# Kernel optimization log

Hardware: AMD Instinct MI355X
Metric: run time of the kernel (lower is better)

Reference implementation:

```python
import jax, jax.numpy as jnp
import numpy as np

N, EG, T, H, EC, L, NT = 10000, 200000, 300000, 128, 128, 3, 100


def _ssp(x):
    # ShiftedSoftplus: softplus(x) - log(2)
    return jax.nn.softplus(x) - jnp.log(2.0).astype(x.dtype)


def _bn(x, g, b):
    # BatchNorm1d in training mode: biased batch stats, eps=1e-5
    m = jnp.mean(x, axis=0)
    v = jnp.var(x, axis=0)
    return g * (x - m) * jax.lax.rsqrt(v + 1e-5) + b


def _forward(z, i, j, idx_i, idx_j, idx_k, idx_ji, idx_kj, pos,
             We1, be1, We2, be2, We3, be3,
             Wc1, bc1, g_c1, b_c1, g_n, b_n,
             Wc2, bc2, g_c2, b_c2, Wc3, bc3, g_c3, b_c3,
             g_c22, b_c22, g_c32, b_c32,
             Wf1, bf1, Wf2, bf2, Wf3, bf3):
    # AtomType2NodeEmb
    h = jax.nn.one_hot(z, NT, dtype=jnp.float32)
    h = _ssp(h @ We1 + be1)
    h = _ssp(h @ We2 + be2)
    node = h @ We3 + be3                      # [N, H]
    # geometry + GaussianFilter edge embedding
    rel = pos[i] - pos[j]                     # [EG, 3]
    dist = jnp.sqrt(jnp.sum(rel * rel, axis=-1))
    unit = rel / dist[:, None]
    offset = jnp.linspace(0.0, 5.0, EC)
    coeff = -0.5 / (offset[1] - offset[0]) ** 2
    edge = jnp.exp(coeff * (dist[:, None] - offset[None, :]) ** 2)  # [EG, EC]
    for l in range(L):
        # NodeUpdate
        c1 = jnp.concatenate([node[i], edge], axis=1) @ Wc1[l] + bc1[l]
        c1 = _bn(c1, g_c1[l], b_c1[l])
        f1, r1 = jnp.split(c1, 2, axis=1)
        agg = jax.ops.segment_sum(jax.nn.sigmoid(f1) * jnp.tanh(r1), i, num_segments=N)
        node = jnp.tanh(node + _bn(agg, g_n[l], b_n[l]))
        # EdgeUpdate: pair term
        c2 = (node[i] * node[j]) @ Wc2[l] + bc2[l]
        c2 = _bn(c2, g_c2[l], b_c2[l])
        f2, r2 = jnp.split(c2, 2, axis=1)
        c2_emb = _bn(jax.nn.sigmoid(f2) * jnp.tanh(r2), g_c22[l], b_c22[l])
        # EdgeUpdate: triplet term
        c3 = jnp.concatenate([node[idx_i], node[idx_j], node[idx_k],
                              edge[idx_ji], edge[idx_kj]], axis=1) @ Wc3[l] + bc3[l]
        c3 = _bn(c3, g_c3[l], b_c3[l])
        f3, r3 = jnp.split(c3, 2, axis=1)
        agg3 = jax.ops.segment_sum(jax.nn.sigmoid(f3) * jnp.tanh(r3), idx_ji, num_segments=EG)
        c3_emb = _bn(agg3, g_c32[l], b_c32[l])
        edge = jnp.tanh(edge + c2_emb + c3_emb)
    # ForcePredictor
    f = _ssp(edge @ Wf1 + bf1)
    f = _ssp(f @ Wf2 + bf2)
    force = (f @ Wf3 + bf3) * unit            # [EG, 3]
    return jax.ops.segment_sum(force, i, num_segments=N)


def setup_inputs() -> dict:
    ks = iter(jax.random.split(jax.random.key(0), 32))

    def w(shape):
        return jax.random.normal(next(ks), shape, jnp.float32) * (shape[-2] ** -0.5)

    z = jax.random.randint(next(ks), (N,), 0, NT)
    pos = jax.random.uniform(next(ks), (N, 3), jnp.float32) * 5.0
    i = jax.random.randint(next(ks), (EG,), 0, N)
    j = (i + 1 + jax.random.randint(next(ks), (EG,), 0, N - 1)) % N  # no self-loops
    idx_i = jax.random.randint(next(ks), (T,), 0, N)
    idx_j = jax.random.randint(next(ks), (T,), 0, N)
    idx_k = jax.random.randint(next(ks), (T,), 0, N)
    idx_ji = jax.random.randint(next(ks), (T,), 0, EG)
    idx_kj = jax.random.randint(next(ks), (T,), 0, EG)
    return dict(
        z=z, pos=pos, i=i, j=j, idx_i=idx_i, idx_j=idx_j, idx_k=idx_k,
        idx_ji=idx_ji, idx_kj=idx_kj,
        We1=w((NT, H)), be1=jnp.zeros((H,)), We2=w((H, H)), be2=jnp.zeros((H,)),
        We3=w((H, H)), be3=jnp.zeros((H,)),
        Wc1=w((L, H + EC, 2 * H)), bc1=jnp.zeros((L, 2 * H)),
        g_c1=jnp.ones((L, 2 * H)), b_c1=jnp.zeros((L, 2 * H)),
        g_n=jnp.ones((L, H)), b_n=jnp.zeros((L, H)),
        Wc2=w((L, H, 2 * EC)), bc2=jnp.zeros((L, 2 * EC)),
        g_c2=jnp.ones((L, 2 * EC)), b_c2=jnp.zeros((L, 2 * EC)),
        Wc3=w((L, 3 * H + 2 * EC, 2 * EC)), bc3=jnp.zeros((L, 2 * EC)),
        g_c3=jnp.ones((L, 2 * EC)), b_c3=jnp.zeros((L, 2 * EC)),
        g_c22=jnp.ones((L, EC)), b_c22=jnp.zeros((L, EC)),
        g_c32=jnp.ones((L, EC)), b_c32=jnp.zeros((L, EC)),
        Wf1=w((EC, EC)), bf1=jnp.zeros((EC,)), Wf2=w((EC, EC)), bf2=jnp.zeros((EC,)),
        Wf3=w((EC, 1)), bf3=jnp.zeros((1,)),
    )


def reference(z, pos, i, j, idx_i, idx_j, idx_k, idx_ji, idx_kj,
              We1, be1, We2, be2, We3, be3,
              Wc1, bc1, g_c1, b_c1, g_n, b_n,
              Wc2, bc2, g_c2, b_c2, Wc3, bc3, g_c3, b_c3,
              g_c22, b_c22, g_c32, b_c32,
              Wf1, bf1, Wf2, bf2, Wf3, bf3):
    return _forward(z, i, j, idx_i, idx_j, idx_k, idx_ji, idx_kj, pos,
                    We1, be1, We2, be2, We3, be3,
                    Wc1, bc1, g_c1, b_c1, g_n, b_n,
                    Wc2, bc2, g_c2, b_c2, Wc3, bc3, g_c3, b_c3,
                    g_c22, b_c22, g_c32, b_c32,
                    Wf1, bf1, Wf2, bf2, Wf3, bf3)
```

## Files before the change

### kernel.cpp

```cpp
#include <hip/hip_runtime.h>

typedef unsigned short u16;
typedef unsigned int   u32;
typedef __attribute__((ext_vector_type(8))) short short8;
typedef __attribute__((ext_vector_type(4))) float f32x4;

#define NN  10000
#define EGN 200000
#define TTN 300000
#define LLN 3

__device__ __forceinline__ float b2f(u16 u){ union{u32 i; float f;} x; x.i=(u32)u<<16; return x.f; }
__device__ __forceinline__ u16 f2b(float f){ union{float f; u32 u;} x; x.f=f; u32 r=(x.u + 0x7fffu + ((x.u>>16)&1u))>>16; return (u16)r; }
__device__ __forceinline__ float sigf(float x){ return 1.f/(1.f+__expf(-x)); }
__device__ __forceinline__ float tanhf_(float x){ float e=__expf(2.f*x); return 1.f - 2.f/(e+1.f); }
__device__ __forceinline__ float sspf(float x){ return fmaxf(x,0.f) + log1pf(__expf(-fabsf(x))) - 0.6931471805599453f; }

__device__ __forceinline__ void async16(void* lds, const void* g){
  __builtin_amdgcn_global_load_lds((const __attribute__((address_space(1))) void*)g,
                                   (__attribute__((address_space(3))) void*)lds, 16, 0, 0);
}
__device__ __forceinline__ void split_store(float v, u16* ph, u16* pl, size_t o){
  u16 h = f2b(v); ph[o] = h; pl[o] = f2b(v - b2f(h));
}
__device__ __forceinline__ short8 ldfragW(const u16* P, int row, int lane){
  int kg = lane>>4;
  int slot = kg ^ ((row>>1)&3);
  return *(const short8*)(P + row*32 + slot*8);
}

struct Segs {
  const u16* sh[10];
  const u16* sl[10];
  const int* idx[10];
  int coff[10];
};

template<int NP>
__device__ __forceinline__ void stageA_W(u16* Ah, u16* Al,
    const u16* sh, const u16* sl, const int* idxp, int co,
    int rb, int M, int tid){
  int row = tid>>2, s = tid&3;
  int kg = s ^ ((row>>1)&3);
  int grow = rb + row; if (grow >= M) grow = M-1;
  int srow = idxp ? idxp[grow] : grow;
  size_t go = (size_t)srow*256 + co + kg*16;
  async16(Ah + tid*8, (const char*)sh + go);
  if (NP==2) async16(Al + tid*8, (const char*)sl + go);
}

template<int NP>
__device__ __forceinline__ void stageA_prod_W(u16* Ah, u16* Al,
    const u16* nh, const u16* nl, const int* pii, const int* pjj,
    int rb, int M, int c2k, int tid){
  int row = tid>>2, q = tid&3;
  int kg = q ^ ((row>>1)&3);
  int e = rb + row; if (e >= M) e = M-1;
  int ia = pii[e], ja = pjj[e];
  size_t boff = c2k*32 + kg*8;
  short8 hi = *(const short8*)(nh + (size_t)ia*128 + boff);
  short8 li = *(const short8*)(nl + (size_t)ia*128 + boff);
  short8 hj = *(const short8*)(nh + (size_t)ja*128 + boff);
  short8 lj = *(const short8*)(nl + (size_t)ja*128 + boff);
  short8 vh, vl;
#pragma unroll
  for (int k=0;k<8;k++){
    float a = b2f((u16)hi[k]) + b2f((u16)li[k]);
    float b = b2f((u16)hj[k]) + b2f((u16)lj[k]);
    float v = a*b;
    u16 h = f2b(v);
    vh[k] = (short)h;
    vl[k] = (short)f2b(v - b2f(h));
  }
  *(short8*)(Ah + row*32 + q*8) = vh;
  if (NP==2) *(short8*)(Al + row*32 + q*8) = vl;
}

template<int NP, int BROWS>
__device__ __forceinline__ void stageB_idW(u16* Bh, u16* Bl,
    const u16* Wh, const u16* Wl, int K2b, int ksoff, int tid){
#pragma unroll
  for (int rnd=0; rnd<BROWS/64; ++rnd){
    int u = rnd*256 + tid;
    int row = u>>2, s = u&3;
    int kg = s ^ ((row>>1)&3);
    size_t go = (size_t)row*K2b + ksoff + kg*16;
    async16(Bh + u*8, (const char*)Wh + go);
    if (NP==2) async16(Bl + u*8, (const char*)Wl + go);
  }
}

template<int NP>
__device__ __forceinline__ void stageB_pairW(u16* Bh, u16* Bl,
    const u16* Wh, const u16* Wl, int P0, int K2b, int ksoff, int tid){
#pragma unroll
  for (int rnd=0; rnd<2; ++rnd){
    int u = rnd*256 + tid;
    int row = u>>2, s = u&3;
    int kg = s ^ ((row>>1)&3);
    int wr = (row < 64) ? (P0 + row) : (128 + P0 + (row-64));
    size_t go = (size_t)wr*K2b + ksoff + kg*16;
    async16(Bh + u*8, (const char*)Wh + go);
    if (NP==2) async16(Bl + u*8, (const char*)Wl + go);
  }
}

template<bool PROD>
__global__ __launch_bounds__(256) void gemm_stats(
  int M, int nseg, Segs segs,
  const u16* __restrict__ nh, const u16* __restrict__ nl,
  const int* __restrict__ pii, const int* __restrict__ pjj,
  const u16* __restrict__ Wh, int K2b, const float* __restrict__ bias,
  float* __restrict__ st)
{
  __shared__ u16 Ah[64*32];
  __shared__ u16 Bh[256*32];
  __shared__ float ls[256], lq[256];
  const int tid = threadIdx.x, lane = tid&63, wv = tid>>6;
  const int lane15 = lane&15;
  const int rb = blockIdx.x*64;
  ls[tid]=0.f; lq[tid]=0.f;

  f32x4 acc[4][4];
#pragma unroll
  for (int m=0;m<4;m++)
#pragma unroll
    for (int n=0;n<4;n++) acc[m][n] = (f32x4){0.f,0.f,0.f,0.f};

  for (int ks=0; ks<nseg; ++ks){
#pragma unroll
    for (int sub=0; sub<2; ++sub){
      if (PROD) stageA_prod_W<1>(Ah, nullptr, nh, nl, pii, pjj, rb, M, ks*2+sub, tid);
      else      stageA_W<1>(Ah, nullptr, segs.sh[ks], nullptr, segs.idx[ks],
                            segs.coff[ks] + sub*64, rb, M, tid);
      stageB_idW<1,256>(Bh, nullptr, Wh, nullptr, K2b, ks*128 + sub*64, tid);
      __syncthreads();
      short8 a[4];
#pragma unroll
      for (int m=0;m<4;m++) a[m] = ldfragW(Ah, m*16 + lane15, lane);
#pragma unroll
      for (int n=0;n<4;n++){
        short8 b = ldfragW(Bh, wv*64 + n*16 + lane15, lane);
#pragma unroll
        for (int m=0;m<4;m++)
          acc[m][n] = __builtin_amdgcn_mfma_f32_16x16x32_bf16(a[m], b, acc[m][n], 0,0,0);
      }
      __syncthreads();
    }
  }
#pragma unroll
  for (int n=0;n<4;n++){
    int col = wv*64 + n*16 + lane15;
    float bb = bias[col];
    float s=0.f, q=0.f;
#pragma unroll
    for (int m=0;m<4;m++){
#pragma unroll
      for (int r=0;r<4;r++){
        int grow = rb + m*16 + (lane>>4)*4 + r;
        if (grow < M){ float v = acc[m][n][r] + bb; s += v; q += v*v; }
      }
    }
    s += __shfl_xor(s,16); s += __shfl_xor(s,32);
    q += __shfl_xor(q,16); q += __shfl_xor(q,32);
    if (lane < 16){ atomicAdd(&ls[wv*64 + n*16 + lane], s); atomicAdd(&lq[wv*64 + n*16 + lane], q); }
  }
  __syncthreads();
  atomicAdd(&st[tid], ls[tid]); atomicAdd(&st[256+tid], lq[tid]);
}

template<int NP, bool PROD, int EPI>
__global__ __launch_bounds__(256) void gemm_pair(
  int M, int nseg, Segs segs,
  const u16* __restrict__ nh, const u16* __restrict__ nl,
  const int* __restrict__ pii, const int* __restrict__ pjj,
  const u16* __restrict__ Wh, const u16* __restrict__ Wl, int K2b,
  const float* __restrict__ bias,
  const float* __restrict__ st, const float* __restrict__ g, const float* __restrict__ b, float inv,
  const int* __restrict__ sidx, float* __restrict__ aggout,
  const float* __restrict__ st22, const float* __restrict__ g22, const float* __restrict__ b22,
  const float* __restrict__ st32, const float* __restrict__ g32, const float* __restrict__ b32, float inv2,
  const float* __restrict__ agg3, u16* __restrict__ eh, u16* __restrict__ el,
  float* __restrict__ st22out)
{
  __shared__ u16 Ah[64*32];
  __shared__ u16 Al[NP==2 ? 64*32 : 32];
  __shared__ u16 Bh[128*32];
  __shared__ u16 Bl[NP==2 ? 128*32 : 32];
  __shared__ float ls[64], lq[64];
  __shared__ float sAf[64], sCf[64], sAr[64], sCr[64];
  __shared__ float sA22[64], sC22[64], sA32[64], sC32[64];
  const int tid = threadIdx.x, lane = tid&63, wv = tid>>6;
  const int lane15 = lane&15;
  const int rb = blockIdx.x*64, P0 = blockIdx.y*64;

  if (tid < 64){
    int p = P0 + tid;
    float m1 = st[p]*inv,     v1 = st[256+p]*inv - m1*m1;
    float a1 = g[p]*rsqrtf(v1+1e-5f);
    sAf[tid]=a1; sCf[tid]=b[p]-a1*m1;
    float m2 = st[128+p]*inv, v2 = st[384+p]*inv - m2*m2;
    float a2 = g[128+p]*rsqrtf(v2+1e-5f);
    sAr[tid]=a2; sCr[tid]=b[128+p]-a2*m2;
    if (EPI==1){
      float m3 = st22[p]*inv2, v3 = st22[128+p]*inv2 - m3*m3;
      float a3 = g22[p]*rsqrtf(v3+1e-5f);
      sA22[tid]=a3; sC22[tid]=b22[p]-a3*m3;
      float m4 = st32[p]*inv2, v4 = st32[128+p]*inv2 - m4*m4;
      float a4 = g32[p]*rsqrtf(v4+1e-5f);
      sA32[tid]=a4; sC32[tid]=b32[p]-a4*m4;
    }
    if (EPI==2){ ls[tid]=0.f; lq[tid]=0.f; }
  }

  f32x4 accf[4], accr[4];
#pragma unroll
  for (int m=0;m<4;m++){ accf[m]=(f32x4){0.f,0.f,0.f,0.f}; accr[m]=(f32x4){0.f,0.f,0.f,0.f}; }

  for (int ks=0; ks<nseg; ++ks){
#pragma unroll
    for (int sub=0; sub<2; ++sub){
      if (PROD) stageA_prod_W<NP>(Ah, Al, nh, nl, pii, pjj, rb, M, ks*2+sub, tid);
      else      stageA_W<NP>(Ah, Al, segs.sh[ks], segs.sl[ks], segs.idx[ks],
                             segs.coff[ks] + sub*64, rb, M, tid);
      stageB_pairW<NP>(Bh, Bl, Wh, Wl, P0, K2b, ks*128 + sub*64, tid);
      __syncthreads();
      short8 ah[4], al[4];
#pragma unroll
      for (int m=0;m<4;m++){
        ah[m] = ldfragW(Ah, m*16 + lane15, lane);
        if constexpr (NP==2) al[m] = ldfragW(Al, m*16 + lane15, lane);
      }
      short8 bfh = ldfragW(Bh, wv*16 + lane15, lane);
      short8 brh = ldfragW(Bh, 64 + wv*16 + lane15, lane);
      short8 bfl, brl;
      if constexpr (NP==2){
        bfl = ldfragW(Bl, wv*16 + lane15, lane);
        brl = ldfragW(Bl, 64 + wv*16 + lane15, lane);
      }
#pragma unroll
      for (int m=0;m<4;m++){
        accf[m] = __builtin_amdgcn_mfma_f32_16x16x32_bf16(ah[m], bfh, accf[m], 0,0,0);
        accr[m] = __builtin_amdgcn_mfma_f32_16x16x32_bf16(ah[m], brh, accr[m], 0,0,0);
        if constexpr (NP==2){
          accf[m] = __builtin_amdgcn_mfma_f32_16x16x32_bf16(ah[m], bfl, accf[m], 0,0,0);
          accf[m] = __builtin_amdgcn_mfma_f32_16x16x32_bf16(al[m], bfh, accf[m], 0,0,0);
          accr[m] = __builtin_amdgcn_mfma_f32_16x16x32_bf16(ah[m], brl, accr[m], 0,0,0);
          accr[m] = __builtin_amdgcn_mfma_f32_16x16x32_bf16(al[m], brh, accr[m], 0,0,0);
        }
      }
      __syncthreads();
    }
  }

  const int pp = wv*16 + lane15;
  const int p  = P0 + pp;
  const float bf_ = bias[p], br_ = bias[128+p];
  const float Af = sAf[pp], Cf = sCf[pp], Ar = sAr[pp], Cr = sCr[pp];
  float su=0.f, sq=0.f;
#pragma unroll
  for (int m=0;m<4;m++){
#pragma unroll
    for (int r=0;r<4;r++){
      int grow = rb + m*16 + (lane>>4)*4 + r;
      if (grow >= M) continue;
      float yf = accf[m][r] + bf_;
      float yr = accr[m][r] + br_;
      float u = sigf(Af*yf + Cf) * tanhf_(Ar*yr + Cr);
      if (EPI==0){
        atomicAdd(&aggout[(size_t)sidx[grow]*128 + p], u);
      } else if (EPI==1){
        size_t o = (size_t)grow*128 + p;
        float eo = b2f(eh[o]) + b2f(el[o]);
        float v = tanhf_(eo + sA22[pp]*u + sC22[pp] + sA32[pp]*agg3[o] + sC32[pp]);
        split_store(v, eh, el, o);
      } else {
        su += u; sq += u*u;
      }
    }
  }
  if (EPI==2){
    su += __shfl_xor(su,16); su += __shfl_xor(su,32);
    sq += __shfl_xor(sq,16); sq += __shfl_xor(sq,32);
    if (lane < 16){ atomicAdd(&ls[wv*16+lane], su); atomicAdd(&lq[wv*16+lane], sq); }
    __syncthreads();
    if (tid < 64){ atomicAdd(&st22out[P0+tid], ls[tid]); atomicAdd(&st22out[128+P0+tid], lq[tid]); }
  }
}

__global__ __launch_bounds__(256) void gemm_force(
  int M, Segs segs,
  const u16* __restrict__ Wh, const u16* __restrict__ Wl, int K2b,
  const float* __restrict__ bias, u16* __restrict__ oh, u16* __restrict__ ol)
{
  __shared__ u16 Ah[64*32], Al[64*32];
  __shared__ u16 Bh[128*32], Bl[128*32];
  const int tid = threadIdx.x, lane = tid&63, wv = tid>>6;
  const int lane15 = lane&15;
  const int rb = blockIdx.x*64;

  f32x4 acc[4][2];
#pragma unroll
  for (int m=0;m<4;m++)
#pragma unroll
    for (int n=0;n<2;n++) acc[m][n] = (f32x4){0.f,0.f,0.f,0.f};

  for (int ks=0; ks<2; ++ks){
#pragma unroll
    for (int sub=0; sub<2; ++sub){
      stageA_W<2>(Ah, Al, segs.sh[ks], segs.sl[ks], segs.idx[ks],
                  segs.coff[ks] + sub*64, rb, M, tid);
      stageB_idW<2,128>(Bh, Bl, Wh, Wl, K2b, ks*128 + sub*64, tid);
      __syncthreads();
      short8 ah[4], al[4];
#pragma unroll
      for (int m=0;m<4;m++){
        ah[m] = ldfragW(Ah, m*16 + lane15, lane);
        al[m] = ldfragW(Al, m*16 + lane15, lane);
      }
#pragma unroll
      for (int n=0;n<2;n++){
        short8 bh = ldfragW(Bh, wv*32 + n*16 + lane15, lane);
        short8 bl = ldfragW(Bl, wv*32 + n*16 + lane15, lane);
#pragma unroll
        for (int m=0;m<4;m++){
          acc[m][n] = __builtin_amdgcn_mfma_f32_16x16x32_bf16(ah[m], bh, acc[m][n], 0,0,0);
          acc[m][n] = __builtin_amdgcn_mfma_f32_16x16x32_bf16(ah[m], bl, acc[m][n], 0,0,0);
          acc[m][n] = __builtin_amdgcn_mfma_f32_16x16x32_bf16(al[m], bh, acc[m][n], 0,0,0);
        }
      }
      __syncthreads();
    }
  }
#pragma unroll
  for (int n=0;n<2;n++){
    int col = wv*32 + n*16 + lane15;
    float bb = bias[col];
#pragma unroll
    for (int m=0;m<4;m++){
#pragma unroll
      for (int r=0;r<4;r++){
        int grow = rb + m*16 + (lane>>4)*4 + r;
        if (grow < M){
          float v = sspf(acc[m][n][r] + bb);
          split_store(v, oh, ol, (size_t)grow*128 + col);
        }
      }
    }
  }
}

__global__ void transpose_cvt(const float* __restrict__ src, u16* __restrict__ dh, u16* __restrict__ dl, int K, int N){
  __shared__ float t[32][33];
  const float* s = src + (size_t)blockIdx.z * K * N;
  u16* dsth = dh + (size_t)blockIdx.z * K * N;
  u16* dstl = dl + (size_t)blockIdx.z * K * N;
  int n0 = blockIdx.x*32, k0 = blockIdx.y*32;
  for (int dy=threadIdx.y; dy<32; dy+=8){
    int k = k0+dy, n = n0+threadIdx.x;
    if (k<K && n<N) t[dy][threadIdx.x] = s[(size_t)k*N + n];
  }
  __syncthreads();
  for (int dy=threadIdx.y; dy<32; dy+=8){
    int n = n0+dy, k = k0+threadIdx.x;
    if (n<N && k<K) split_store(t[threadIdx.x][dy], dsth, dstl, (size_t)n*K + k);
  }
}

__global__ __launch_bounds__(128) void embed_k(const int* __restrict__ z,
  const float* __restrict__ We1, const float* __restrict__ be1,
  const float* __restrict__ We2, const float* __restrict__ be2,
  const float* __restrict__ We3, const float* __restrict__ be3,
  u16* __restrict__ nh, u16* __restrict__ nl){
  __shared__ float h0[128], h1[128];
  int nid = blockIdx.x, t = threadIdx.x;
  int zz = z[nid];
  h0[t] = sspf(We1[zz*128 + t] + be1[t]);
  __syncthreads();
  float a = be2[t];
  for (int k=0;k<128;k++) a += h0[k]*We2[k*128+t];
  h1[t] = sspf(a);
  __syncthreads();
  float b = be3[t];
  for (int k=0;k<128;k++) b += h1[k]*We3[k*128+t];
  split_store(b, nh, nl, (size_t)nid*128+t);
}

__global__ __launch_bounds__(256) void geom_k(const float* __restrict__ pos,
  const int* __restrict__ ii, const int* __restrict__ jj,
  float* __restrict__ unitv, u16* __restrict__ eh, u16* __restrict__ el){
  int t = threadIdx.x; int e = blockIdx.x*2 + (t>>7); int col = t&127;
  int a = ii[e], b = jj[e];
  float dx = pos[a*3]-pos[b*3], dy=pos[a*3+1]-pos[b*3+1], dz=pos[a*3+2]-pos[b*3+2];
  float dist = sqrtf(dx*dx+dy*dy+dz*dz);
  if (col==0){ float inv=1.f/dist; unitv[e*3]=dx*inv; unitv[e*3+1]=dy*inv; unitv[e*3+2]=dz*inv; }
  const float step = 5.0f/127.0f;
  const float coeff = -0.5f/(step*step);
  float d = dist - step*(float)col;
  float g = __expf(coeff*d*d);
  split_store(g, eh, el, (size_t)e*128+col);
}

__global__ __launch_bounds__(256) void colstats128(const float* __restrict__ m, int M, float* __restrict__ st){
  __shared__ float ls[128], lq[128];
  int t=threadIdx.x; if(t<128){ls[t]=0.f;lq[t]=0.f;} __syncthreads();
  int col=t&127, hf=t>>7; float ps=0.f,pq=0.f;
  int npair=(M+1)>>1;
  for (int pr=blockIdx.x; pr<npair; pr+=gridDim.x){
    int row=pr*2+hf;
    if(row<M){ float v=m[(size_t)row*128+col]; ps+=v; pq+=v*v; }
  }
  atomicAdd(&ls[col],ps); atomicAdd(&lq[col],pq);
  __syncthreads();
  if(t<128){ atomicAdd(&st[t],ls[t]); atomicAdd(&st[128+t],lq[t]); }
}

__global__ __launch_bounds__(256) void node_update_k(u16* __restrict__ nh, u16* __restrict__ nl,
  const float* __restrict__ agg, const float* __restrict__ st,
  const float* __restrict__ g, const float* __restrict__ b, float inv, int Nn)
{
  int t=threadIdx.x; int col=t&127, hf=t>>7;
  float mean = st[col]*inv;
  float var  = st[128+col]*inv - mean*mean;
  float A = g[col]*rsqrtf(var+1e-5f);
  float C = b[col] - A*mean;
  int npair=(Nn+1)>>1;
  for (int pr=blockIdx.x; pr<npair; pr+=gridDim.x){
    int row=pr*2+hf; if(row>=Nn) continue;
    size_t o=(size_t)row*128+col;
    float nv = b2f(nh[o]) + b2f(nl[o]);
    float v = tanhf_(nv + A*agg[o] + C);
    split_store(v, nh, nl, o);
  }
}

__global__ __launch_bounds__(256) void force_k(const u16* __restrict__ fh, const u16* __restrict__ fl,
  const float* __restrict__ Wf3, const float* __restrict__ bf3,
  const float* __restrict__ unitv, const int* __restrict__ ii, float* __restrict__ outp, int Me)
{
  int wv=threadIdx.x>>6, lane=threadIdx.x&63;
  int e = blockIdx.x*4 + wv; if(e>=Me) return;
  size_t o0=(size_t)e*128+lane, o1=o0+64;
  float p = (b2f(fh[o0])+b2f(fl[o0]))*Wf3[lane] + (b2f(fh[o1])+b2f(fl[o1]))*Wf3[64+lane];
  for (int s=32;s>0;s>>=1) p += __shfl_down(p, s);
  if (lane==0){
    float F = p + bf3[0];
    atomicAdd(&outp[ii[e]*3+0], F*unitv[e*3+0]);
    atomicAdd(&outp[ii[e]*3+1], F*unitv[e*3+1]);
    atomicAdd(&outp[ii[e]*3+2], F*unitv[e*3+2]);
  }
}

__global__ void sentinel_k(float* o, int n, float v){
  int i = blockIdx.x*256 + threadIdx.x; if (i<n) o[i]=v;
}

extern "C" void kernel_launch(void* const* d_in, const int* in_sizes, int n_in,
                              void* d_out, int out_size, void* d_ws, size_t ws_size,
                              hipStream_t stream)
{
  (void)in_sizes; (void)n_in;
  const int* z      = (const int*)d_in[0];
  const float* pos  = (const float*)d_in[1];
  const int* ii     = (const int*)d_in[2];
  const int* jj     = (const int*)d_in[3];
  const int* idx_i  = (const int*)d_in[4];
  const int* idx_j  = (const int*)d_in[5];
  const int* idx_k  = (const int*)d_in[6];
  const int* idx_ji = (const int*)d_in[7];
  const int* idx_kj = (const int*)d_in[8];
  const float* We1=(const float*)d_in[9];  const float* be1=(const float*)d_in[10];
  const float* We2=(const float*)d_in[11]; const float* be2=(const float*)d_in[12];
  const float* We3=(const float*)d_in[13]; const float* be3=(const float*)d_in[14];
  const float* Wc1=(const float*)d_in[15]; const float* bc1=(const float*)d_in[16];
  const float* g_c1=(const float*)d_in[17]; const float* b_c1=(const float*)d_in[18];
  const float* g_n=(const float*)d_in[19]; const float* b_n=(const float*)d_in[20];
  const float* Wc2=(const float*)d_in[21]; const float* bc2=(const float*)d_in[22];
  const float* g_c2=(const float*)d_in[23]; const float* b_c2=(const float*)d_in[24];
  const float* Wc3=(const float*)d_in[25]; const float* bc3=(const float*)d_in[26];
  const float* g_c3=(const float*)d_in[27]; const float* b_c3=(const float*)d_in[28];
  const float* g_c22=(const float*)d_in[29]; const float* b_c22=(const float*)d_in[30];
  const float* g_c32=(const float*)d_in[31]; const float* b_c32=(const float*)d_in[32];
  const float* Wf1=(const float*)d_in[33]; const float* bf1=(const float*)d_in[34];
  const float* Wf2=(const float*)d_in[35]; const float* bf2=(const float*)d_in[36];
  const float* Wf3=(const float*)d_in[37]; const float* bf3=(const float*)d_in[38];

  char* ws = (char*)d_ws;
  size_t off=0;
  auto alloc=[&](size_t bb){ size_t o=off; off += (bb+255)&~(size_t)255; return o; };
  u16*   node_h = (u16*)(ws + alloc((size_t)NN*128*2));
  u16*   node_l = (u16*)(ws + alloc((size_t)NN*128*2));
  u16*   edge_h = (u16*)(ws + alloc((size_t)EGN*128*2));
  u16*   edge_l = (u16*)(ws + alloc((size_t)EGN*128*2));
  float* unitv  = (float*)(ws + alloc((size_t)EGN*3*4));
  float* agg    = (float*)(ws + alloc((size_t)NN*128*4));
  float* agg3   = (float*)(ws + alloc((size_t)EGN*128*4));
  u16*   wc1h   = (u16*)(ws + alloc((size_t)3*256*256*2));
  u16*   wc1l   = (u16*)(ws + alloc((size_t)3*256*256*2));
  u16*   wc2h   = (u16*)(ws + alloc((size_t)3*256*128*2));
  u16*   wc2l   = (u16*)(ws + alloc((size_t)3*256*128*2));
  u16*   wc3h   = (u16*)(ws + alloc((size_t)3*256*640*2));
  u16*   wc3l   = (u16*)(ws + alloc((size_t)3*256*640*2));
  u16*   wf1h   = (u16*)(ws + alloc((size_t)128*128*2));
  u16*   wf1l   = (u16*)(ws + alloc((size_t)128*128*2));
  u16*   wf2h   = (u16*)(ws + alloc((size_t)128*128*2));
  u16*   wf2l   = (u16*)(ws + alloc((size_t)128*128*2));
  float* stats  = (float*)(ws + alloc(2304*4));

  if (off > ws_size){
    sentinel_k<<<(out_size+255)/256, 256, 0, stream>>>((float*)d_out, out_size, 123456.0f);
    return;
  }

  float* st1 = stats;
  float* st2 = stats+512;
  float* st3 = stats+1024;
  float* stN = stats+1536;
  float* st32= stats+1792;
  float* st22= stats+2048;

  u16* f1h = (u16*)agg3;
  u16* f1l = f1h + (size_t)EGN*128;
  u16* f2h = edge_h;
  u16* f2l = edge_l;

  hipMemsetAsync(d_out, 0, (size_t)out_size*4, stream);

  dim3 tb(32,8);
  transpose_cvt<<<dim3(8,8,3),  tb, 0, stream>>>(Wc1, wc1h, wc1l, 256, 256);
  transpose_cvt<<<dim3(8,4,3),  tb, 0, stream>>>(Wc2, wc2h, wc2l, 128, 256);
  transpose_cvt<<<dim3(8,20,3), tb, 0, stream>>>(Wc3, wc3h, wc3l, 640, 256);
  transpose_cvt<<<dim3(4,4,1),  tb, 0, stream>>>(Wf1, wf1h, wf1l, 128, 128);
  transpose_cvt<<<dim3(4,4,1),  tb, 0, stream>>>(Wf2, wf2h, wf2l, 128, 128);

  embed_k<<<NN,128,0,stream>>>(z, We1,be1,We2,be2,We3,be3, node_h, node_l);
  geom_k<<<EGN/2,256,0,stream>>>(pos, ii, jj, unitv, edge_h, edge_l);

  const int gE64  = (EGN+63)/64;
  const int gT64  = (TTN+63)/64;
  Segs dummy{};
  const float invE = 1.0f/EGN, invT = 1.0f/TTN, invN = 1.0f/NN;

  for (int l=0;l<LLN;l++){
    hipMemsetAsync(stats, 0, 2304*4, stream);
    hipMemsetAsync(agg,  0, (size_t)NN*128*4, stream);
    hipMemsetAsync(agg3, 0, (size_t)EGN*128*4, stream);

    const u16* w1h = wc1h + l*256*256; const u16* w1l = wc1l + l*256*256;
    const u16* w2h = wc2h + l*256*128; const u16* w2l = wc2l + l*256*128;
    const u16* w3h = wc3h + l*256*640; const u16* w3l = wc3l + l*256*640;

    Segs s1{};
    s1.sh[0]=node_h; s1.sl[0]=node_l; s1.idx[0]=ii;      s1.coff[0]=0;
    s1.sh[1]=node_h; s1.sl[1]=node_l; s1.idx[1]=ii;      s1.coff[1]=128;
    s1.sh[2]=edge_h; s1.sl[2]=edge_l; s1.idx[2]=nullptr; s1.coff[2]=0;
    s1.sh[3]=edge_h; s1.sl[3]=edge_l; s1.idx[3]=nullptr; s1.coff[3]=128;
    gemm_stats<false><<<gE64,256,0,stream>>>(EGN, 4, s1, nullptr,nullptr,nullptr,nullptr,
                                             w1h, 512, bc1+l*256, st1);
    gemm_pair<2,false,0><<<dim3(gE64,2),256,0,stream>>>(EGN, 4, s1, nullptr,nullptr,nullptr,nullptr,
        w1h, w1l, 512, bc1+l*256,
        st1, g_c1+l*256, b_c1+l*256, invE,
        ii, agg,
        nullptr,nullptr,nullptr, nullptr,nullptr,nullptr, 0.f,
        nullptr, nullptr, nullptr, nullptr);
    colstats128<<<256,256,0,stream>>>(agg, NN, stN);
    node_update_k<<<2048,256,0,stream>>>(node_h, node_l, agg, stN, g_n+l*128, b_n+l*128, invN, NN);

    Segs s3{};
    s3.sh[0]=node_h; s3.sl[0]=node_l; s3.idx[0]=idx_i;  s3.coff[0]=0;
    s3.sh[1]=node_h; s3.sl[1]=node_l; s3.idx[1]=idx_i;  s3.coff[1]=128;
    s3.sh[2]=node_h; s3.sl[2]=node_l; s3.idx[2]=idx_j;  s3.coff[2]=0;
    s3.sh[3]=node_h; s3.sl[3]=node_l; s3.idx[3]=idx_j;  s3.coff[3]=128;
    s3.sh[4]=node_h; s3.sl[4]=node_l; s3.idx[4]=idx_k;  s3.coff[4]=0;
    s3.sh[5]=node_h; s3.sl[5]=node_l; s3.idx[5]=idx_k;  s3.coff[5]=128;
    s3.sh[6]=edge_h; s3.sl[6]=edge_l; s3.idx[6]=idx_ji; s3.coff[6]=0;
    s3.sh[7]=edge_h; s3.sl[7]=edge_l; s3.idx[7]=idx_ji; s3.coff[7]=128;
    s3.sh[8]=edge_h; s3.sl[8]=edge_l; s3.idx[8]=idx_kj; s3.coff[8]=0;
    s3.sh[9]=edge_h; s3.sl[9]=edge_l; s3.idx[9]=idx_kj; s3.coff[9]=128;
    gemm_stats<false><<<gT64,256,0,stream>>>(TTN, 10, s3, nullptr,nullptr,nullptr,nullptr,
                                             w3h, 1280, bc3+l*256, st3);
    gemm_pair<2,false,0><<<dim3(gT64,2),256,0,stream>>>(TTN, 10, s3, nullptr,nullptr,nullptr,nullptr,
        w3h, w3l, 1280, bc3+l*256,
        st3, g_c3+l*256, b_c3+l*256, invT,
        idx_ji, agg3,
        nullptr,nullptr,nullptr, nullptr,nullptr,nullptr, 0.f,
        nullptr, nullptr, nullptr, nullptr);
    colstats128<<<1024,256,0,stream>>>(agg3, EGN, st32);

    gemm_stats<true><<<gE64,256,0,stream>>>(EGN, 2, dummy, node_h,node_l,ii,jj,
                                            w2h, 256, bc2+l*256, st2);
    gemm_pair<1,true,2><<<dim3(gE64,2),256,0,stream>>>(EGN, 2, dummy, node_h,node_l,ii,jj,
        w2h, nullptr, 256, bc2+l*256,
        st2, g_c2+l*256, b_c2+l*256, invE,
        nullptr, nullptr,
        nullptr,nullptr,nullptr, nullptr,nullptr,nullptr, 0.f,
        nullptr, nullptr, nullptr, st22);
    gemm_pair<2,true,1><<<dim3(gE64,2),256,0,stream>>>(EGN, 2, dummy, node_h,node_l,ii,jj,
        w2h, w2l, 256, bc2+l*256,
        st2, g_c2+l*256, b_c2+l*256, invE,
        nullptr, nullptr,
        st22, g_c22+l*128, b_c22+l*128, st32, g_c32+l*128, b_c32+l*128, invE,
        agg3, edge_h, edge_l, nullptr);
  }

  Segs sf1{}; sf1.sh[0]=edge_h; sf1.sl[0]=edge_l; sf1.idx[0]=nullptr; sf1.coff[0]=0;
              sf1.sh[1]=edge_h; sf1.sl[1]=edge_l; sf1.idx[1]=nullptr; sf1.coff[1]=128;
  gemm_force<<<gE64,256,0,stream>>>(EGN, sf1, wf1h, wf1l, 256, bf1, f1h, f1l);
  Segs sf2{}; sf2.sh[0]=f1h; sf2.sl[0]=f1l; sf2.idx[0]=nullptr; sf2.coff[0]=0;
              sf2.sh[1]=f1h; sf2.sl[1]=f1l; sf2.idx[1]=nullptr; sf2.coff[1]=128;
  gemm_force<<<gE64,256,0,stream>>>(EGN, sf2, wf2h, wf2l, 256, bf2, f2h, f2l);
  force_k<<<(EGN+3)/4,256,0,stream>>>(f2h, f2l, Wf3, bf3, unitv, ii, (float*)d_out, EGN);
}
```

Baseline: 4.327 ms.

## Load GEMM operand fragments directly from global memory instead of staging through LDS

All GEMM kernels (stats, pair, force) stop staging A and B tiles through shared memory with async global-to-LDS loads and barriers. Each lane now loads its MFMA fragments straight from global memory, with gather row indices precomputed once per kernel, and the loops are fully unrolled over sources and k-steps. This removes the per-step __syncthreads and LDS traffic. In exchange, weight fragments are reloaded redundantly by every wave and block instead of being shared, the loads are narrower and less coalesced, and unrolling raises register pressure.

```diff
diff --git a/kernel.cpp b/kernel.cpp
--- a/kernel.cpp
+++ b/kernel.cpp
@@ -16,53 +16,21 @@
 __device__ __forceinline__ float tanhf_(float x){ float e=__expf(2.f*x); return 1.f - 2.f/(e+1.f); }
 __device__ __forceinline__ float sspf(float x){ return fmaxf(x,0.f) + log1pf(__expf(-fabsf(x))) - 0.6931471805599453f; }
 
-__device__ __forceinline__ void async16(void* lds, const void* g){
-  __builtin_amdgcn_global_load_lds((const __attribute__((address_space(1))) void*)g,
-                                   (__attribute__((address_space(3))) void*)lds, 16, 0, 0);
-}
 __device__ __forceinline__ void split_store(float v, u16* ph, u16* pl, size_t o){
   u16 h = f2b(v); ph[o] = h; pl[o] = f2b(v - b2f(h));
 }
-__device__ __forceinline__ short8 ldfragW(const u16* P, int row, int lane){
-  int kg = lane>>4;
-  int slot = kg ^ ((row>>1)&3);
-  return *(const short8*)(P + row*32 + slot*8);
-}
-
-struct Segs {
-  const u16* sh[10];
-  const u16* sl[10];
-  const int* idx[10];
-  int coff[10];
-};
-
-template<int NP>
-__device__ __forceinline__ void stageA_W(u16* Ah, u16* Al,
-    const u16* sh, const u16* sl, const int* idxp, int co,
-    int rb, int M, int tid){
-  int row = tid>>2, s = tid&3;
-  int kg = s ^ ((row>>1)&3);
-  int grow = rb + row; if (grow >= M) grow = M-1;
-  int srow = idxp ? idxp[grow] : grow;
-  size_t go = (size_t)srow*256 + co + kg*16;
-  async16(Ah + tid*8, (const char*)sh + go);
-  if (NP==2) async16(Al + tid*8, (const char*)sl + go);
-}
-
-template<int NP>
-__device__ __forceinline__ void stageA_prod_W(u16* Ah, u16* Al,
-    const u16* nh, const u16* nl, const int* pii, const int* pjj,
-    int rb, int M, int c2k, int tid){
-  int row = tid>>2, q = tid&3;
-  int kg = q ^ ((row>>1)&3);
-  int e = rb + row; if (e >= M) e = M-1;
-  int ia = pii[e], ja = pjj[e];
-  size_t boff = c2k*32 + kg*8;
-  short8 hi = *(const short8*)(nh + (size_t)ia*128 + boff);
-  short8 li = *(const short8*)(nl + (size_t)ia*128 + boff);
-  short8 hj = *(const short8*)(nh + (size_t)ja*128 + boff);
-  short8 lj = *(const short8*)(nl + (size_t)ja*128 + boff);
-  short8 vh, vl;
+__device__ __forceinline__ short8 ldA(const u16* p, int srow, int chunk){
+  return *(const short8*)(p + (size_t)srow*128 + chunk*8);
+}
+__device__ __forceinline__ short8 ldBd(const u16* W, int row, int K2u, int chunk){
+  return *(const short8*)(W + (size_t)row*K2u + chunk*8);
+}
+__device__ __forceinline__ void prodfrag(const u16* nh, const u16* nl, int ri, int rj, int chunk,
+                                         short8& vh, short8& vl){
+  short8 hi = *(const short8*)(nh + (size_t)ri*128 + chunk*8);
+  short8 li = *(const short8*)(nl + (size_t)ri*128 + chunk*8);
+  short8 hj = *(const short8*)(nh + (size_t)rj*128 + chunk*8);
+  short8 lj = *(const short8*)(nl + (size_t)rj*128 + chunk*8);
 #pragma unroll
   for (int k=0;k<8;k++){
     float a = b2f((u16)hi[k]) + b2f((u16)li[k]);
@@ -72,82 +40,73 @@
     vh[k] = (short)h;
     vl[k] = (short)f2b(v - b2f(h));
   }
-  *(short8*)(Ah + row*32 + q*8) = vh;
-  if (NP==2) *(short8*)(Al + row*32 + q*8) = vl;
-}
-
-template<int NP, int BROWS>
-__device__ __forceinline__ void stageB_idW(u16* Bh, u16* Bl,
-    const u16* Wh, const u16* Wl, int K2b, int ksoff, int tid){
-#pragma unroll
-  for (int rnd=0; rnd<BROWS/64; ++rnd){
-    int u = rnd*256 + tid;
-    int row = u>>2, s = u&3;
-    int kg = s ^ ((row>>1)&3);
-    size_t go = (size_t)row*K2b + ksoff + kg*16;
-    async16(Bh + u*8, (const char*)Wh + go);
-    if (NP==2) async16(Bl + u*8, (const char*)Wl + go);
-  }
-}
-
-template<int NP>
-__device__ __forceinline__ void stageB_pairW(u16* Bh, u16* Bl,
-    const u16* Wh, const u16* Wl, int P0, int K2b, int ksoff, int tid){
-#pragma unroll
-  for (int rnd=0; rnd<2; ++rnd){
-    int u = rnd*256 + tid;
-    int row = u>>2, s = u&3;
-    int kg = s ^ ((row>>1)&3);
-    int wr = (row < 64) ? (P0 + row) : (128 + P0 + (row-64));
-    size_t go = (size_t)wr*K2b + ksoff + kg*16;
-    async16(Bh + u*8, (const char*)Wh + go);
-    if (NP==2) async16(Bl + u*8, (const char*)Wl + go);
-  }
-}
-
-template<bool PROD>
+}
+
+struct Segs {
+  const u16* sh[5];
+  const u16* sl[5];
+  const int* idx[5];
+};
+
+template<int NSRC, bool PROD>
 __global__ __launch_bounds__(256) void gemm_stats(
-  int M, int nseg, Segs segs,
+  int M, Segs segs,
   const u16* __restrict__ nh, const u16* __restrict__ nl,
   const int* __restrict__ pii, const int* __restrict__ pjj,
-  const u16* __restrict__ Wh, int K2b, const float* __restrict__ bias,
+  const u16* __restrict__ Wh, const float* __restrict__ bias,
   float* __restrict__ st)
 {
-  __shared__ u16 Ah[64*32];
-  __shared__ u16 Bh[256*32];
   __shared__ float ls[256], lq[256];
   const int tid = threadIdx.x, lane = tid&63, wv = tid>>6;
-  const int lane15 = lane&15;
+  const int lane15 = lane&15, kg = lane>>4;
   const int rb = blockIdx.x*64;
+  const int K2u = NSRC*128;
   ls[tid]=0.f; lq[tid]=0.f;
 
+  int srI[4], srJ[4];
+  int srow[NSRC][4];
+#pragma unroll
+  for (int m=0;m<4;m++){
+    int grow = rb + m*16 + lane15; if (grow >= M) grow = M-1;
+    if (PROD){ srI[m]=pii[grow]; srJ[m]=pjj[grow]; }
+    else {
+#pragma unroll
+      for (int s=0;s<NSRC;s++) srow[s][m] = segs.idx[s] ? segs.idx[s][grow] : grow;
+    }
+  }
+
   f32x4 acc[4][4];
 #pragma unroll
   for (int m=0;m<4;m++)
 #pragma unroll
     for (int n=0;n<4;n++) acc[m][n] = (f32x4){0.f,0.f,0.f,0.f};
 
-  for (int ks=0; ks<nseg; ++ks){
-#pragma unroll
-    for (int sub=0; sub<2; ++sub){
-      if (PROD) stageA_prod_W<1>(Ah, nullptr, nh, nl, pii, pjj, rb, M, ks*2+sub, tid);
-      else      stageA_W<1>(Ah, nullptr, segs.sh[ks], nullptr, segs.idx[ks],
-                            segs.coff[ks] + sub*64, rb, M, tid);
-      stageB_idW<1,256>(Bh, nullptr, Wh, nullptr, K2b, ks*128 + sub*64, tid);
-      __syncthreads();
+#pragma unroll
+  for (int s=0;s<NSRC;s++){
+#pragma unroll
+    for (int stp=0;stp<4;stp++){
+      const int ch = stp*4 + kg;
+      const int bch = s*16 + ch;
       short8 a[4];
-#pragma unroll
-      for (int m=0;m<4;m++) a[m] = ldfragW(Ah, m*16 + lane15, lane);
-#pragma unroll
-      for (int n=0;n<4;n++){
-        short8 b = ldfragW(Bh, wv*64 + n*16 + lane15, lane);
+      if (PROD){
+#pragma unroll
+        for (int m=0;m<4;m++){ short8 vl_; prodfrag(nh,nl,srI[m],srJ[m],ch,a[m],vl_); }
+      } else {
+#pragma unroll
+        for (int m=0;m<4;m++) a[m] = ldA(segs.sh[s], srow[s][m], ch);
+      }
+      short8 b[4];
+#pragma unroll
+      for (int n=0;n<4;n++) b[n] = ldBd(Wh, wv*64 + n*16 + lane15, K2u, bch);
+#pragma unroll
+      for (int n=0;n<4;n++)
 #pragma unroll
         for (int m=0;m<4;m++)
-          acc[m][n] = __builtin_amdgcn_mfma_f32_16x16x32_bf16(a[m], b, acc[m][n], 0,0,0);
-      }
-      __syncthreads();
-    }
-  }
+          acc[m][n] = __builtin_amdgcn_mfma_f32_16x16x32_bf16(a[m], b[n], acc[m][n], 0,0,0);
+    }
+  }
+
+  __syncthreads();
 #pragma unroll
   for (int n=0;n<4;n++){
     int col = wv*64 + n*16 + lane15;
@@ -169,12 +128,12 @@
   atomicAdd(&st[tid], ls[tid]); atomicAdd(&st[256+tid], lq[tid]);
 }
 
-template<int NP, bool PROD, int EPI>
+template<int NSRC, int NP, bool PROD, int EPI>
 __global__ __launch_bounds__(256) void gemm_pair(
-  int M, int nseg, Segs segs,
+  int M, Segs segs,
   const u16* __restrict__ nh, const u16* __restrict__ nl,
   const int* __restrict__ pii, const int* __restrict__ pjj,
-  const u16* __restrict__ Wh, const u16* __restrict__ Wl, int K2b,
+  const u16* __restrict__ Wh, const u16* __restrict__ Wl,
   const float* __restrict__ bias,
   const float* __restrict__ st, const float* __restrict__ g, const float* __restrict__ b, float inv,
   const int* __restrict__ sidx, float* __restrict__ aggout,
@@ -183,16 +142,13 @@
   const float* __restrict__ agg3, u16* __restrict__ eh, u16* __restrict__ el,
   float* __restrict__ st22out)
 {
-  __shared__ u16 Ah[64*32];
-  __shared__ u16 Al[NP==2 ? 64*32 : 32];
-  __shared__ u16 Bh[128*32];
-  __shared__ u16 Bl[NP==2 ? 128*32 : 32];
   __shared__ float ls[64], lq[64];
   __shared__ float sAf[64], sCf[64], sAr[64], sCr[64];
   __shared__ float sA22[64], sC22[64], sA32[64], sC32[64];
   const int tid = threadIdx.x, lane = tid&63, wv = tid>>6;
-  const int lane15 = lane&15;
+  const int lane15 = lane&15, kg = lane>>4;
   const int rb = blockIdx.x*64, P0 = blockIdx.y*64;
+  const int K2u = NSRC*128;
 
   if (tid < 64){
     int p = P0 + tid;
@@ -213,46 +169,60 @@
     if (EPI==2){ ls[tid]=0.f; lq[tid]=0.f; }
   }
 
+  int srI[4], srJ[4];
+  int srow[NSRC][4];
+#pragma unroll
+  for (int m=0;m<4;m++){
+    int grow = rb + m*16 + lane15; if (grow >= M) grow = M-1;
+    if (PROD){ srI[m]=pii[grow]; srJ[m]=pjj[grow]; }
+    else {
+#pragma unroll
+      for (int s=0;s<NSRC;s++) srow[s][m] = segs.idx[s] ? segs.idx[s][grow] : grow;
+    }
+  }
+  const int bRowF = P0 + wv*16 + lane15;
+  const int bRowR = 128 + bRowF;
+
   f32x4 accf[4], accr[4];
 #pragma unroll
   for (int m=0;m<4;m++){ accf[m]=(f32x4){0.f,0.f,0.f,0.f}; accr[m]=(f32x4){0.f,0.f,0.f,0.f}; }
 
-  for (int ks=0; ks<nseg; ++ks){
-#pragma unroll
-    for (int sub=0; sub<2; ++sub){
-      if (PROD) stageA_prod_W<NP>(Ah, Al, nh, nl, pii, pjj, rb, M, ks*2+sub, tid);
-      else      stageA_W<NP>(Ah, Al, segs.sh[ks], segs.sl[ks], segs.idx[ks],
-                             segs.coff[ks] + sub*64, rb, M, tid);
-      stageB_pairW<NP>(Bh, Bl, Wh, Wl, P0, K2b, ks*128 + sub*64, tid);
-      __syncthreads();
+#pragma unroll
+  for (int s=0;s<NSRC;s++){
+#pragma unroll
+    for (int stp=0;stp<4;stp++){
+      const int ch = stp*4 + kg;
+      const int bch = s*16 + ch;
       short8 ah[4], al[4];
-#pragma unroll
-      for (int m=0;m<4;m++){
-        ah[m] = ldfragW(Ah, m*16 + lane15, lane);
-        if constexpr (NP==2) al[m] = ldfragW(Al, m*16 + lane15, lane);
-      }
-      short8 bfh = ldfragW(Bh, wv*16 + lane15, lane);
-      short8 brh = ldfragW(Bh, 64 + wv*16 + lane15, lane);
+      if (PROD){
+#pragma unroll
+        for (int m=0;m<4;m++) prodfrag(nh,nl,srI[m],srJ[m],ch,ah[m],al[m]);
+      } else {
+#pragma unroll
+        for (int m=0;m<4;m++){
+          ah[m] = ldA(segs.sh[s], srow[s][m], ch);
+          if (NP==2) al[m] = ldA(segs.sl[s], srow[s][m], ch);
+        }
+      }
+      short8 bfh = ldBd(Wh, bRowF, K2u, bch);
+      short8 brh = ldBd(Wh, bRowR, K2u, bch);
       short8 bfl, brl;
-      if constexpr (NP==2){
-        bfl = ldfragW(Bl, wv*16 + lane15, lane);
-        brl = ldfragW(Bl, 64 + wv*16 + lane15, lane);
-      }
+      if (NP==2){ bfl = ldBd(Wl, bRowF, K2u, bch); brl = ldBd(Wl, bRowR, K2u, bch); }
 #pragma unroll
       for (int m=0;m<4;m++){
         accf[m] = __builtin_amdgcn_mfma_f32_16x16x32_bf16(ah[m], bfh, accf[m], 0,0,0);
         accr[m] = __builtin_amdgcn_mfma_f32_16x16x32_bf16(ah[m], brh, accr[m], 0,0,0);
-        if constexpr (NP==2){
+        if (NP==2){
           accf[m] = __builtin_amdgcn_mfma_f32_16x16x32_bf16(ah[m], bfl, accf[m], 0,0,0);
           accf[m] = __builtin_amdgcn_mfma_f32_16x16x32_bf16(al[m], bfh, accf[m], 0,0,0);
           accr[m] = __builtin_amdgcn_mfma_f32_16x16x32_bf16(ah[m], brl, accr[m], 0,0,0);
           accr[m] = __builtin_amdgcn_mfma_f32_16x16x32_bf16(al[m], brh, accr[m], 0,0,0);
         }
       }
-      __syncthreads();
-    }
-  }
-
+    }
+  }
+
+  __syncthreads();
   const int pp = wv*16 + lane15;
   const int p  = P0 + pp;
   const float bf_ = bias[p], br_ = bias[128+p];
@@ -289,47 +259,46 @@
 }
 
 __global__ __launch_bounds__(256) void gemm_force(
-  int M, Segs segs,
-  const u16* __restrict__ Wh, const u16* __restrict__ Wl, int K2b,
+  int M, const u16* __restrict__ Ahp, const u16* __restrict__ Alp,
+  const u16* __restrict__ Wh, const u16* __restrict__ Wl,
   const float* __restrict__ bias, u16* __restrict__ oh, u16* __restrict__ ol)
 {
-  __shared__ u16 Ah[64*32], Al[64*32];
-  __shared__ u16 Bh[128*32], Bl[128*32];
   const int tid = threadIdx.x, lane = tid&63, wv = tid>>6;
-  const int lane15 = lane&15;
+  const int lane15 = lane&15, kg = lane>>4;
   const int rb = blockIdx.x*64;
 
+  int srow[4];
+#pragma unroll
+  for (int m=0;m<4;m++){
+    int grow = rb + m*16 + lane15; if (grow >= M) grow = M-1;
+    srow[m] = grow;
+  }
+
   f32x4 acc[4][2];
 #pragma unroll
   for (int m=0;m<4;m++)
 #pragma unroll
     for (int n=0;n<2;n++) acc[m][n] = (f32x4){0.f,0.f,0.f,0.f};
 
-  for (int ks=0; ks<2; ++ks){
-#pragma unroll
-    for (int sub=0; sub<2; ++sub){
-      stageA_W<2>(Ah, Al, segs.sh[ks], segs.sl[ks], segs.idx[ks],
-                  segs.coff[ks] + sub*64, rb, M, tid);
-      stageB_idW<2,128>(Bh, Bl, Wh, Wl, K2b, ks*128 + sub*64, tid);
-      __syncthreads();
-      short8 ah[4], al[4];
+#pragma unroll
+  for (int stp=0;stp<4;stp++){
+    const int ch = stp*4 + kg;
+    short8 ah[4], al[4];
+#pragma unroll
+    for (int m=0;m<4;m++){
+      ah[m] = ldA(Ahp, srow[m], ch);
+      al[m] = ldA(Alp, srow[m], ch);
+    }
+#pragma unroll
+    for (int n=0;n<2;n++){
+      short8 bh = ldBd(Wh, wv*32 + n*16 + lane15, 128, ch);
+      short8 bl = ldBd(Wl, wv*32 + n*16 + lane15, 128, ch);
 #pragma unroll
       for (int m=0;m<4;m++){
-        ah[m] = ldfragW(Ah, m*16 + lane15, lane);
-        al[m] = ldfragW(Al, m*16 + lane15, lane);
-      }
-#pragma unroll
-      for (int n=0;n<2;n++){
-        short8 bh = ldfragW(Bh, wv*32 + n*16 + lane15, lane);
-        short8 bl = ldfragW(Bl, wv*32 + n*16 + lane15, lane);
-#pragma unroll
-        for (int m=0;m<4;m++){
-          acc[m][n] = __builtin_amdgcn_mfma_f32_16x16x32_bf16(ah[m], bh, acc[m][n], 0,0,0);
-          acc[m][n] = __builtin_amdgcn_mfma_f32_16x16x32_bf16(ah[m], bl, acc[m][n], 0,0,0);
-          acc[m][n] = __builtin_amdgcn_mfma_f32_16x16x32_bf16(al[m], bh, acc[m][n], 0,0,0);
-        }
-      }
-      __syncthreads();
+        acc[m][n] = __builtin_amdgcn_mfma_f32_16x16x32_bf16(ah[m], bh, acc[m][n], 0,0,0);
+        acc[m][n] = __builtin_amdgcn_mfma_f32_16x16x32_bf16(ah[m], bl, acc[m][n], 0,0,0);
+        acc[m][n] = __builtin_amdgcn_mfma_f32_16x16x32_bf16(al[m], bh, acc[m][n], 0,0,0);
+      }
     }
   }
 #pragma unroll
@@ -551,14 +520,12 @@
     const u16* w3h = wc3h + l*256*640; const u16* w3l = wc3l + l*256*640;
 
     Segs s1{};
-    s1.sh[0]=node_h; s1.sl[0]=node_l; s1.idx[0]=ii;      s1.coff[0]=0;
-    s1.sh[1]=node_h; s1.sl[1]=node_l; s1.idx[1]=ii;      s1.coff[1]=128;
-    s1.sh[2]=edge_h; s1.sl[2]=edge_l; s1.idx[2]=nullptr; s1.coff[2]=0;
-    s1.sh[3]=edge_h; s1.sl[3]=edge_l; s1.idx[3]=nullptr; s1.coff[3]=128;
-    gemm_stats<false><<<gE64,256,0,stream>>>(EGN, 4, s1, nullptr,nullptr,nullptr,nullptr,
-                                             w1h, 512, bc1+l*256, st1);
-    gemm_pair<2,false,0><<<dim3(gE64,2),256,0,stream>>>(EGN, 4, s1, nullptr,nullptr,nullptr,nullptr,
-        w1h, w1l, 512, bc1+l*256,
+    s1.sh[0]=node_h; s1.sl[0]=node_l; s1.idx[0]=ii;
+    s1.sh[1]=edge_h; s1.sl[1]=edge_l; s1.idx[1]=nullptr;
+    gemm_stats<2,false><<<gE64,256,0,stream>>>(EGN, s1, nullptr,nullptr,nullptr,nullptr,
+                                               w1h, bc1+l*256, st1);
+    gemm_pair<2,2,false,0><<<dim3(gE64,2),256,0,stream>>>(EGN, s1, nullptr,nullptr,nullptr,nullptr,
+        w1h, w1l, bc1+l*256,
         st1, g_c1+l*256, b_c1+l*256, invE,
         ii, agg,
         nullptr,nullptr,nullptr, nullptr,nullptr,nullptr, 0.f,
@@ -567,47 +534,38 @@
     node_update_k<<<2048,256,0,stream>>>(node_h, node_l, agg, stN, g_n+l*128, b_n+l*128, invN, NN);
 
     Segs s3{};
-    s3.sh[0]=node_h; s3.sl[0]=node_l; s3.idx[0]=idx_i;  s3.coff[0]=0;
-    s3.sh[1]=node_h; s3.sl[1]=node_l; s3.idx[1]=idx_i;  s3.coff[1]=128;
-    s3.sh[2]=node_h; s3.sl[2]=node_l; s3.idx[2]=idx_j;  s3.coff[2]=0;
-    s3.sh[3]=node_h; s3.sl[3]=node_l; s3.idx[3]=idx_j;  s3.coff[3]=128;
-    s3.sh[4]=node_h; s3.sl[4]=node_l; s3.idx[4]=idx_k;  s3.coff[4]=0;
-    s3.sh[5]=node_h; s3.sl[5]=node_l; s3.idx[5]=idx_k;  s3.coff[5]=128;
-    s3.sh[6]=edge_h; s3.sl[6]=edge_l; s3.idx[6]=idx_ji; s3.coff[6]=0;
-    s3.sh[7]=edge_h; s3.sl[7]=edge_l; s3.idx[7]=idx_ji; s3.coff[7]=128;
-    s3.sh[8]=edge_h; s3.sl[8]=edge_l; s3.idx[8]=idx_kj; s3.coff[8]=0;
-    s3.sh[9]=edge_h; s3.sl[9]=edge_l; s3.idx[9]=idx_kj; s3.coff[9]=128;
-    gemm_stats<false><<<gT64,256,0,stream>>>(TTN, 10, s3, nullptr,nullptr,nullptr,nullptr,
-                                             w3h, 1280, bc3+l*256, st3);
-    gemm_pair<2,false,0><<<dim3(gT64,2),256,0,stream>>>(TTN, 10, s3, nullptr,nullptr,nullptr,nullptr,
-        w3h, w3l, 1280, bc3+l*256,
+    s3.sh[0]=node_h; s3.sl[0]=node_l; s3.idx[0]=idx_i;
+    s3.sh[1]=node_h; s3.sl[1]=node_l; s3.idx[1]=idx_j;
+    s3.sh[2]=node_h; s3.sl[2]=node_l; s3.idx[2]=idx_k;
+    s3.sh[3]=edge_h; s3.sl[3]=edge_l; s3.idx[3]=idx_ji;
+    s3.sh[4]=edge_h; s3.sl[4]=edge_l; s3.idx[4]=idx_kj;
+    gemm_stats<5,false><<<gT64,256,0,stream>>>(TTN, s3, nullptr,nullptr,nullptr,nullptr,
+                                               w3h, bc3+l*256, st3);
+    gemm_pair<5,2,false,0><<<dim3(gT64,2),256,0,stream>>>(TTN, s3, nullptr,nullptr,nullptr,nullptr,
+        w3h, w3l, bc3+l*256,
         st3, g_c3+l*256, b_c3+l*256, invT,
         idx_ji, agg3,
         nullptr,nullptr,nullptr, nullptr,nullptr,nullptr, 0.f,
         nullptr, nullptr, nullptr, nullptr);
     colstats128<<<1024,256,0,stream>>>(agg3, EGN, st32);
 
-    gemm_stats<true><<<gE64,256,0,stream>>>(EGN, 2, dummy, node_h,node_l,ii,jj,
-                                            w2h, 256, bc2+l*256, st2);
-    gemm_pair<1,true,2><<<dim3(gE64,2),256,0,stream>>>(EGN, 2, dummy, node_h,node_l,ii,jj,
-        w2h, nullptr, 256, bc2+l*256,
+    gemm_stats<1,true><<<gE64,256,0,stream>>>(EGN, dummy, node_h,node_l,ii,jj,
+                                              w2h, bc2+l*256, st2);
+    gemm_pair<1,1,true,2><<<dim3(gE64,2),256,0,stream>>>(EGN, dummy, node_h,node_l,ii,jj,
+        w2h, nullptr, bc2+l*256,
         st2, g_c2+l*256, b_c2+l*256, invE,
         nullptr, nullptr,
         nullptr,nullptr,nullptr, nullptr,nullptr,nullptr, 0.f,
         nullptr, nullptr, nullptr, st22);
-    gemm_pair<2,true,1><<<dim3(gE64,2),256,0,stream>>>(EGN, 2, dummy, node_h,node_l,ii,jj,
-        w2h, w2l, 256, bc2+l*256,
+    gemm_pair<1,2,true,1><<<dim3(gE64,2),256,0,stream>>>(EGN, dummy, node_h,node_l,ii,jj,
+        w2h, w2l, bc2+l*256,
         st2, g_c2+l*256, b_c2+l*256, invE,
         nullptr, nullptr,
         st22, g_c22+l*128, b_c22+l*128, st32, g_c32+l*128, b_c32+l*128, invE,
         agg3, edge_h, edge_l, nullptr);
   }
 
-  Segs sf1{}; sf1.sh[0]=edge_h; sf1.sl[0]=edge_l; sf1.idx[0]=nullptr; sf1.coff[0]=0;
-              sf1.sh[1]=edge_h; sf1.sl[1]=edge_l; sf1.idx[1]=nullptr; sf1.coff[1]=128;
-  gemm_force<<<gE64,256,0,stream>>>(EGN, sf1, wf1h, wf1l, 256, bf1, f1h, f1l);
-  Segs sf2{}; sf2.sh[0]=f1h; sf2.sl[0]=f1l; sf2.idx[0]=nullptr; sf2.coff[0]=0;
-              sf2.sh[1]=f1h; sf2.sl[1]=f1l; sf2.idx[1]=nullptr; sf2.coff[1]=128;
-  gemm_force<<<gE64,256,0,stream>>>(EGN, sf2, wf2h, wf2l, 256, bf2, f2h, f2l);
+  gemm_force<<<gE64,256,0,stream>>>(EGN, edge_h, edge_l, wf1h, wf1l, bf1, f1h, f1l);
+  gemm_force<<<gE64,256,0,stream>>>(EGN, f1h, f1l, wf2h, wf2l, bf2, f2h, f2l);
   force_k<<<(EGN+3)/4,256,0,stream>>>(f2h, f2l, Wf3, bf3, unitv, ii, (float*)d_out, EGN);
 }
```

Result: slower. 8.540 ms (+97.4%).
